# Performance work log

Hardware: AMD Instinct MI355X
Metric: run time of the kernel (lower is better)

Reference implementation:

```python
import jax, jax.numpy as jnp
import numpy as np

HIDDEN = 3072
N_HEADS = 16
Q_LORA = 1536
KV_LORA = 512
NOPE = 128
ROPE = 64
QK_HD = NOPE + ROPE  # 192
V_HD = 128
B, S = 2, 1024


def rms_norm(x, w, eps=1e-6):
    xf = x.astype(jnp.float32)
    var = jnp.mean(xf * xf, axis=-1, keepdims=True)
    return w * (xf * jax.lax.rsqrt(var + eps)).astype(x.dtype)


def apply_rope(x):
    # x: (b, s, h, d) with d even; interleaved pair rotation as in the source
    b, s, h, d = x.shape
    pos = jnp.arange(s, dtype=jnp.float32)
    inv_freq = 1.0 / (10000.0 ** (jnp.arange(0, d, 2, dtype=jnp.float32) / d))
    ang = pos[:, None] * inv_freq[None, :]          # (s, d/2)
    sin = jnp.sin(ang)[None, :, None, :]            # (1, s, 1, d/2)
    cos = jnp.cos(ang)[None, :, None, :]
    xr = x.reshape(b, s, h, d // 2, 2)
    x1, x2 = xr[..., 0], xr[..., 1]
    r1 = x1 * cos - x2 * sin
    r2 = x1 * sin + x2 * cos
    return jnp.stack([r1, r2], axis=-1).reshape(b, s, h, d)


def setup_inputs() -> dict:
    key = jax.random.key(0)
    ks = jax.random.split(key, 16)
    sc = 0.02
    inp = {
        "hidden_states": jax.random.normal(ks[0], (B, S, HIDDEN), jnp.float32),
        # causal additive mask (s, t): 0 on/below diagonal, -1e9 above
        "mask": jnp.where(jnp.tril(jnp.ones((S, S), bool)), 0.0, -1e9).astype(jnp.float32),
        "wq_a_w": jax.random.normal(ks[1], (Q_LORA, HIDDEN), jnp.float32) * sc,
        "wq_a_b": jnp.zeros((Q_LORA,), jnp.float32),
        "q_norm_w": jnp.ones((Q_LORA,), jnp.float32),
        "wq_b_w": jax.random.normal(ks[2], (HIDDEN, Q_LORA), jnp.float32) * sc,
        "wq_b_b": jnp.zeros((HIDDEN,), jnp.float32),
        "wkv_a_w": jax.random.normal(ks[3], (KV_LORA + ROPE, HIDDEN), jnp.float32) * sc,
        "wkv_a_b": jnp.zeros((KV_LORA + ROPE,), jnp.float32),
        "kv_norm_w": jnp.ones((KV_LORA,), jnp.float32),
        "wkv_b_w": jax.random.normal(ks[4], (N_HEADS * (NOPE + V_HD), KV_LORA), jnp.float32) * sc,
        "wkv_b_b": jnp.zeros((N_HEADS * (NOPE + V_HD),), jnp.float32),
        "wo_w": jax.random.normal(ks[5], (HIDDEN, N_HEADS * V_HD), jnp.float32) * sc,
        "wo_b": jnp.zeros((HIDDEN,), jnp.float32),
    }
    return inp


def reference(hidden_states, mask, wq_a_w, wq_a_b, q_norm_w, wq_b_w, wq_b_b,
              wkv_a_w, wkv_a_b, kv_norm_w, wkv_b_w, wkv_b_b, wo_w, wo_b):
    b, s, _ = hidden_states.shape
    scale = QK_HD ** (-0.5)

    # low-rank Q projection
    q_lat = hidden_states @ wq_a_w.T + wq_a_b                  # (b,s,q_lora)
    q = rms_norm(q_lat, q_norm_w) @ wq_b_w.T + wq_b_b          # (b,s,hidden)
    q = q.reshape(b, s, N_HEADS, QK_HD)
    q_nope, q_rope = q[..., :NOPE], q[..., NOPE:]
    q_rope = apply_rope(q_rope)
    q = jnp.concatenate([q_nope, q_rope], axis=-1)             # (b,s,h,192)

    # low-rank KV projection with decoupled rope key
    kv = hidden_states @ wkv_a_w.T + wkv_a_b                   # (b,s,kv_lora+rope)
    kv_lat, k_rope = kv[..., :KV_LORA], kv[..., KV_LORA:]
    k_rope = apply_rope(k_rope[:, :, None, :])                 # (b,s,1,64)
    kv = rms_norm(kv_lat, kv_norm_w) @ wkv_b_w.T + wkv_b_b
    kv = kv.reshape(b, s, N_HEADS, NOPE + V_HD)
    k_nope, v = kv[..., :NOPE], kv[..., NOPE:]
    k = jnp.concatenate([k_nope, jnp.broadcast_to(k_rope, (b, s, N_HEADS, ROPE))], axis=-1)

    # naive full attention, fp32 softmax (as in source)
    scores = jnp.einsum('bshd,bthd->bsht', q, k) * scale       # (b,s,h,t)
    scores = scores + mask[None, :, None, :]
    p = jax.nn.softmax(scores.astype(jnp.float32), axis=-1)
    out = jnp.einsum('bsht,bthd->bshd', p, v)                  # (b,s,h,v_hd)
    out = out.reshape(b, s, N_HEADS * V_HD)
    return out @ wo_w.T + wo_b
```

## Files before the change

kernel.cpp:

```cpp
#include <hip/hip_runtime.h>
#include <stdint.h>
#include <stddef.h>

#define NHEADS 16
#define QLORA  1536
#define KVLORA 512
#define QKH    192
#define VH     128
#define BB     2
#define SS     1024
#define MROWS  (BB*SS)
#define HID    3072

typedef __attribute__((ext_vector_type(4))) float fx4;
typedef __attribute__((ext_vector_type(4))) short sx4;
typedef __attribute__((ext_vector_type(8))) short sx8;

__device__ __forceinline__ short f2bf(float f) {
  uint32_t u = __builtin_bit_cast(uint32_t, f);
  u = (u + 0x7fffu + ((u >> 16) & 1u)) >> 16;
  return (short)u;
}
__device__ __forceinline__ float bf2f(short s) {
  uint32_t u = ((uint32_t)(uint16_t)s) << 16;
  return __builtin_bit_cast(float, u);
}
__device__ __forceinline__ void gl_lds16(const void* g, void* l) {
  __builtin_amdgcn_global_load_lds((const __attribute__((address_space(1))) void*)g,
                                   (__attribute__((address_space(3))) void*)l, 16, 0, 0);
}
__device__ __forceinline__ sx8 ldfrag(const short* p) {
  sx4 lo = *(const sx4*)p;
  sx4 hi = *(const sx4*)(p + 16);
  sx8 r;
  r[0]=lo[0]; r[1]=lo[1]; r[2]=lo[2]; r[3]=lo[3];
  r[4]=hi[0]; r[5]=hi[1]; r[6]=hi[2]; r[7]=hi[3];
  return r;
}
__device__ __forceinline__ sx8 ldfrag_swz(const short* lds, int row, int rowShorts,
                                          int baseChunk, int g) {
  const int r7 = row & 7;
  const int gh = g >> 1, lo4 = (g & 1) * 4;
  int ch0 = baseChunk + gh;
  int ch1 = baseChunk + 2 + gh;
  ch0 = (ch0 & ~7) | ((ch0 & 7) ^ r7);
  ch1 = (ch1 & ~7) | ((ch1 & 7) ^ r7);
  const short* base = lds + row * rowShorts;
  sx4 a = *(const sx4*)(base + ch0 * 8 + lo4);
  sx4 b = *(const sx4*)(base + ch1 * 8 + lo4);
  sx8 r;
  r[0]=a[0]; r[1]=a[1]; r[2]=a[2]; r[3]=a[3];
  r[4]=b[0]; r[5]=b[1]; r[6]=b[2]; r[7]=b[3];
  return r;
}
__device__ __forceinline__ sx8 ldfrag_swz32(const short* lds, int row, int g) {
  const int f = (row >> 1) & 3;
  const int c0 = (g >> 1) ^ f;
  const int c1 = (2 + (g >> 1)) ^ f;
  const int lo4 = (g & 1) * 4;
  const short* base = lds + row * 32;
  sx4 a = *(const sx4*)(base + c0 * 8 + lo4);
  sx4 b = *(const sx4*)(base + c1 * 8 + lo4);
  sx8 r;
  r[0]=a[0]; r[1]=a[1]; r[2]=a[2]; r[3]=a[3];
  r[4]=b[0]; r[5]=b[1]; r[6]=b[2]; r[7]=b[3];
  return r;
}

struct CvtSeg { const float* src; short* dst; int n4; };
__global__ void k_cvt6(CvtSeg s0, CvtSeg s1, CvtSeg s2, CvtSeg s3, CvtSeg s4, CvtSeg s5) {
  const CvtSeg segs[6] = {s0, s1, s2, s3, s4, s5};
  const int stride = gridDim.x * blockDim.x;
  const int t0 = blockIdx.x * blockDim.x + threadIdx.x;
#pragma unroll
  for (int s = 0; s < 6; ++s) {
    const float* src = segs[s].src;
    short* dst = segs[s].dst;
    const int n4 = segs[s].n4;
    for (int i = t0; i < n4; i += stride) {
      fx4 v = *(const fx4*)(src + (size_t)i * 4);
      sx4 o;
      o[0] = f2bf(v[0]); o[1] = f2bf(v[1]); o[2] = f2bf(v[2]); o[3] = f2bf(v[3]);
      *(sx4*)(dst + (size_t)i * 4) = o;
    }
  }
}

__global__ void k_rope_tab(float* __restrict__ tab) {
  int i = blockIdx.x * blockDim.x + threadIdx.x;
  if (i >= SS * 32) return;
  int pos = i >> 5, fi = i & 31;
  float inv = powf(10000.0f, -(float)fi / 32.0f);
  float ang = (float)pos * inv;
  tab[i * 2]     = cosf(ang);
  tab[i * 2 + 1] = sinf(ang);
}

struct GemmProb {
  const short* A; const short* Bt; const float* bias; void* C;
  int N; int K; int outbf16;
};

template <int MFR>
__global__ __launch_bounds__(256, 3)
void k_gemm2(GemmProb p0, GemmProb p1, int nblk0) {
  constexpr int TM = MFR * 32;
  constexpr int MT = 2048 / TM;
  int nwg = gridDim.x;
  int bid = (blockIdx.x % 8) * (nwg >> 3) + (blockIdx.x >> 3);
  const GemmProb p = (bid < nblk0) ? p0 : p1;
  int lb = (bid < nblk0) ? bid : bid - nblk0;
  const int m0 = (lb % MT) * TM;
  const int n0 = (lb / MT) * 128;

  __shared__ short As[2][TM * 32];
  __shared__ short Bs[2][128 * 32];
  const int tid  = threadIdx.x;
  const int lane = tid & 63;
  const int g    = lane >> 4;
  const int r16  = lane & 15;
  const int wave = tid >> 6;
  const int wm   = (wave >> 1) * (TM / 2);
  const int wn   = (wave & 1) * 64;
  const int N = p.N, K = p.K;

  fx4 acc[MFR][4] = {};

#define STAGE(bufi, kk)                                                        \
  do {                                                                         \
    _Pragma("unroll")                                                          \
    for (int i = 0; i < MFR / 2; ++i) {                                        \
      int cc = tid + 256 * i;                                                  \
      int row = cc >> 2;                                                       \
      int sc = ((cc & 3) ^ (row >> 1)) & 3;                                    \
      gl_lds16(p.A + (size_t)(m0 + row) * K + (kk) + sc * 8,                   \
               &As[bufi][cc * 8]);                                             \
    }                                                                          \
    _Pragma("unroll")                                                          \
    for (int i = 0; i < 2; ++i) {                                              \
      int cc = tid + 256 * i;                                                  \
      int row = cc >> 2;                                                       \
      int sc = ((cc & 3) ^ (row >> 1)) & 3;                                    \
      int bn = n0 + row; if (bn > N - 1) bn = N - 1;                           \
      gl_lds16(p.Bt + (size_t)bn * K + (kk) + sc * 8, &Bs[bufi][cc * 8]);      \
    }                                                                          \
  } while (0)

  const int nk = K >> 5;
  STAGE(0, 0);
  __syncthreads();

  int cur = 0;
  for (int t = 0; t < nk - 1; ++t) {
    STAGE(cur ^ 1, (t + 1) * 32);
    {
      sx8 af[MFR], bfv[4];
#pragma unroll
      for (int mi = 0; mi < MFR; ++mi)
        af[mi] = ldfrag_swz32(&As[cur][0], wm + mi * 16 + r16, g);
#pragma unroll
      for (int ni = 0; ni < 4; ++ni)
        bfv[ni] = ldfrag_swz32(&Bs[cur][0], wn + ni * 16 + r16, g);
#pragma unroll
      for (int mi = 0; mi < MFR; ++mi)
#pragma unroll
        for (int ni = 0; ni < 4; ++ni)
          acc[mi][ni] = __builtin_amdgcn_mfma_f32_16x16x32_bf16(af[mi], bfv[ni], acc[mi][ni], 0, 0, 0);
    }
    __syncthreads();
    cur ^= 1;
  }
  {
    sx8 af[MFR], bfv[4];
#pragma unroll
    for (int mi = 0; mi < MFR; ++mi)
      af[mi] = ldfrag_swz32(&As[cur][0], wm + mi * 16 + r16, g);
#pragma unroll
    for (int ni = 0; ni < 4; ++ni)
      bfv[ni] = ldfrag_swz32(&Bs[cur][0], wn + ni * 16 + r16, g);
#pragma unroll
    for (int mi = 0; mi < MFR; ++mi)
#pragma unroll
      for (int ni = 0; ni < 4; ++ni)
        acc[mi][ni] = __builtin_amdgcn_mfma_f32_16x16x32_bf16(af[mi], bfv[ni], acc[mi][ni], 0, 0, 0);
  }
#undef STAGE

  if (p.outbf16) {
#pragma unroll
    for (int mi = 0; mi < MFR; ++mi) {
      int mbase = m0 + wm + mi * 16 + 4 * g;
#pragma unroll
      for (int ni = 0; ni < 4; ++ni) {
        int ncol = n0 + wn + ni * 16 + r16;
        if (ncol < N) {
          float bv = p.bias[ncol];
#pragma unroll
          for (int r = 0; r < 4; ++r)
            ((short*)p.C)[(size_t)(mbase + r) * N + ncol] = f2bf(acc[mi][ni][r] + bv);
        }
      }
    }
  } else {
#pragma unroll
    for (int mi = 0; mi < MFR; ++mi) {
      int mbase = m0 + wm + mi * 16 + 4 * g;
#pragma unroll
      for (int ni = 0; ni < 4; ++ni) {
        int ncol = n0 + wn + ni * 16 + r16;
        if (ncol < N) {
          float bv = p.bias[ncol];
#pragma unroll
          for (int r = 0; r < 4; ++r)
            ((float*)p.C)[(size_t)(mbase + r) * N + ncol] = acc[mi][ni][r] + bv;
        }
      }
    }
  }
}

__global__ __launch_bounds__(256)
void k_prep(const short* __restrict__ qlat, const float* __restrict__ q_norm_w,
            short* __restrict__ qn,
            const short* __restrict__ kv, const float* __restrict__ kv_norm_w,
            short* __restrict__ kvn, short* __restrict__ kr,
            const float* __restrict__ tab) {
  const int row = blockIdx.x;
  const int t = threadIdx.x;
  const short* qr  = qlat + (size_t)row * QLORA;
  const short* kvr = kv + (size_t)row * 576;

  sx8 v;
  float s1 = 0.f, s2 = 0.f;
  if (t < 192) {
    v = *(const sx8*)(qr + t * 8);
#pragma unroll
    for (int j = 0; j < 8; ++j) { float f = bf2f(v[j]); s1 += f * f; }
  } else {
    v = *(const sx8*)(kvr + (t - 192) * 8);
#pragma unroll
    for (int j = 0; j < 8; ++j) { float f = bf2f(v[j]); s2 += f * f; }
  }
#pragma unroll
  for (int o = 32; o >= 1; o >>= 1) {
    s1 += __shfl_xor(s1, o, 64);
    s2 += __shfl_xor(s2, o, 64);
  }
  __shared__ float r1[4], r2[4];
  if ((t & 63) == 0) { r1[t >> 6] = s1; r2[t >> 6] = s2; }
  __syncthreads();
  float qss = r1[0] + r1[1] + r1[2] + r1[3];
  float kss = r2[0] + r2[1] + r2[2] + r2[3];
  float qrs = 1.0f / sqrtf(qss / (float)QLORA + 1e-6f);
  float krs = 1.0f / sqrtf(kss / (float)KVLORA + 1e-6f);

  if (t < 192) {
    sx8 o;
#pragma unroll
    for (int j = 0; j < 8; ++j) o[j] = f2bf(bf2f(v[j]) * qrs * q_norm_w[t * 8 + j]);
    *(sx8*)(qn + (size_t)row * QLORA + t * 8) = o;
  } else {
    int c = t - 192;
    sx8 o;
#pragma unroll
    for (int j = 0; j < 8; ++j) o[j] = f2bf(bf2f(v[j]) * krs * kv_norm_w[c * 8 + j]);
    *(sx8*)(kvn + (size_t)row * KVLORA + c * 8) = o;
  }
  if (t < 8) {
    sx8 x = *(const sx8*)(kvr + 512 + t * 8);
    int pos = row & (SS - 1);
    sx8 o;
#pragma unroll
    for (int k = 0; k < 4; ++k) {
      int i = t * 4 + k;
      float c = tab[(pos * 32 + i) * 2], s = tab[(pos * 32 + i) * 2 + 1];
      float x1 = bf2f(x[2 * k]), x2 = bf2f(x[2 * k + 1]);
      o[2 * k]     = f2bf(x1 * c - x2 * s);
      o[2 * k + 1] = f2bf(x1 * s + x2 * c);
    }
    *(sx8*)(kr + (size_t)row * 64 + t * 8) = o;
  }
}

__global__ __launch_bounds__(256)
void k_post(const short* __restrict__ kvb, short* __restrict__ vt,
            short* __restrict__ qb, const float* __restrict__ tab) {
  const int bid = blockIdx.x;
  const int tid = threadIdx.x;
  if (bid < 512) {
    const int bh = bid >> 4;
    const int t0 = (bid & 15) * 64;
    const int b = bh >> 4, h = bh & 15;
    __shared__ short sm[64 * 128];
#pragma unroll
    for (int i = 0; i < 4; ++i) {
      int c = tid + 256 * i;
      int tt = c >> 4, d0 = (c & 15) * 8;
      sx8 v = *(const sx8*)(kvb + ((size_t)(b * SS + t0 + tt)) * 4096 + h * 256 + 128 + d0);
      *(sx8*)(sm + tt * 128 + d0) = v;
    }
    __syncthreads();
#pragma unroll
    for (int i = 0; i < 4; ++i) {
      int c = tid + 256 * i;
      int d = c >> 3, tof = (c & 7) * 8;
      sx8 v;
#pragma unroll
      for (int j = 0; j < 8; ++j) v[j] = sm[(tof + j) * 128 + d];
      *(sx8*)(vt + ((size_t)bh * VH + d) * SS + t0 + tof) = v;
    }
  } else {
    int p = (bid - 512) * 256 + tid;
    int j = p & 7, h = (p >> 3) & 15, row = p >> 7;
    int pos = row & (SS - 1);
    size_t base = (((size_t)row * NHEADS + h) * QKH) + 128 + j * 8;
    sx8 x = *(const sx8*)(qb + base);
    sx8 o;
#pragma unroll
    for (int k = 0; k < 4; ++k) {
      int i = j * 4 + k;
      float c = tab[(pos * 32 + i) * 2], s = tab[(pos * 32 + i) * 2 + 1];
      float x1 = bf2f(x[2 * k]), x2 = bf2f(x[2 * k + 1]);
      o[2 * k]     = f2bf(x1 * c - x2 * s);
      o[2 * k + 1] = f2bf(x1 * s + x2 * c);
    }
    *(sx8*)(qb + base) = o;
  }
}

__global__ __launch_bounds__(256, 2)
void k_attn(const short* __restrict__ q, const short* __restrict__ kvb,
            const short* __restrict__ kr, const short* __restrict__ vt,
            short* __restrict__ ao) {
  const int bh = blockIdx.x;
  const int b = bh >> 4, h = bh & 15;
  const int qt0 = blockIdx.y * 64;
  const int tid = threadIdx.x;
  const int lane = tid & 63;
  const int wave = tid >> 6;
  const int g = lane >> 4, r16 = lane & 15;
  const int qg = qt0 + wave * 16 + r16;

  __shared__ short Ks[64 * QKH];
  __shared__ short Vs[VH * 64];

  sx8 qf[6];
  {
    const short* qr = q + (((size_t)(b * SS + qg)) * NHEADS + h) * QKH;
#pragma unroll
    for (int f = 0; f < 6; ++f) qf[f] = ldfrag(qr + f * 32 + 4 * g);
  }

  float mrun = -1e30f, lrun = 0.0f;
  fx4 oacc[8] = {};
  const float scale = 0.07216878364870323f;

  const int ntiles = qt0 / 64 + 1;
  for (int kt = 0; kt < ntiles; ++kt) {
    const int t0 = kt * 64;
#pragma unroll
    for (int i = 0; i < 6; ++i) {
      int cc = tid + 256 * i;
      int row = cc / 24, ch = cc % 24;
      int sc = (ch & 24) | ((ch & 7) ^ (row & 7));
      size_t grow = (size_t)(b * SS + t0 + row);
      const short* src = (sc < 16) ? kvb + grow * 4096 + h * 256 + sc * 8
                                   : kr + grow * 64 + (sc - 16) * 8;
      gl_lds16(src, &Ks[cc * 8]);
    }
#pragma unroll
    for (int i = 0; i < 4; ++i) {
      int cc = tid + 256 * i;
      int row = cc >> 3;
      int sc = (cc & 7) ^ (row & 7);
      gl_lds16(vt + ((size_t)bh * VH + row) * SS + t0 + sc * 8, &Vs[cc * 8]);
    }
    __syncthreads();

    const bool diag = (kt == ntiles - 1);
    float pv[16];
    float tmax = -1e30f;
#pragma unroll
    for (int th = 0; th < 4; ++th) {
      fx4 sacc = {};
#pragma unroll
      for (int f = 0; f < 6; ++f) {
        sx8 kf = ldfrag_swz(Ks, th * 16 + r16, QKH, f * 4, g);
        sacc = __builtin_amdgcn_mfma_f32_16x16x32_bf16(kf, qf[f], sacc, 0, 0, 0);
      }
#pragma unroll
      for (int r = 0; r < 4; ++r) {
        int t = t0 + th * 16 + 4 * g + r;
        float s = sacc[r] * scale;
        if (diag && t > qg) s = -1e30f;
        pv[th * 4 + r] = s;
        tmax = fmaxf(tmax, s);
      }
    }
    tmax = fmaxf(tmax, __shfl_xor(tmax, 16, 64));
    tmax = fmaxf(tmax, __shfl_xor(tmax, 32, 64));
    float mnew = fmaxf(mrun, tmax);
    float corr = __expf(mrun - mnew);
    float psum = 0.f;
#pragma unroll
    for (int j = 0; j < 16; ++j) { pv[j] = __expf(pv[j] - mnew); psum += pv[j]; }
    psum += __shfl_xor(psum, 16, 64);
    psum += __shfl_xor(psum, 32, 64);
    lrun = lrun * corr + psum;
    mrun = mnew;
#pragma unroll
    for (int f8 = 0; f8 < 8; ++f8) oacc[f8] *= corr;

    sx8 pf0, pf1;
#pragma unroll
    for (int j = 0; j < 8; ++j) { pf0[j] = f2bf(pv[j]); pf1[j] = f2bf(pv[8 + j]); }

#pragma unroll
    for (int f8 = 0; f8 < 8; ++f8) {
      sx8 v0 = ldfrag_swz(Vs, f8 * 16 + r16, 64, 0, g);
      sx8 v1 = ldfrag_swz(Vs, f8 * 16 + r16, 64, 4, g);
      oacc[f8] = __builtin_amdgcn_mfma_f32_16x16x32_bf16(v0, pf0, oacc[f8], 0, 0, 0);
      oacc[f8] = __builtin_amdgcn_mfma_f32_16x16x32_bf16(v1, pf1, oacc[f8], 0, 0, 0);
    }
    __syncthreads();
  }

  float inv = 1.0f / lrun;
#pragma unroll
  for (int f8 = 0; f8 < 8; ++f8)
#pragma unroll
    for (int r = 0; r < 4; ++r) {
      int d = f8 * 16 + 4 * g + r;
      ao[(((size_t)(b * SS + qg)) * NHEADS + h) * VH + d] = f2bf(oacc[f8][r] * inv);
    }
}

extern "C" void kernel_launch(void* const* d_in, const int* in_sizes, int n_in,
                              void* d_out, int out_size, void* d_ws, size_t ws_size,
                              hipStream_t stream) {
  const float* hs       = (const float*)d_in[0];
  const float* wq_a_w   = (const float*)d_in[2];
  const float* wq_a_b   = (const float*)d_in[3];
  const float* q_norm_w = (const float*)d_in[4];
  const float* wq_b_w   = (const float*)d_in[5];
  const float* wq_b_b   = (const float*)d_in[6];
  const float* wkv_a_w  = (const float*)d_in[7];
  const float* wkv_a_b  = (const float*)d_in[8];
  const float* kv_norm_w= (const float*)d_in[9];
  const float* wkv_b_w  = (const float*)d_in[10];
  const float* wkv_b_b  = (const float*)d_in[11];
  const float* wo_w     = (const float*)d_in[12];
  const float* wo_b     = (const float*)d_in[13];
  float* out = (float*)d_out;

  short* ws0 = (short*)d_ws;
  size_t off = 0;
  short* wqa_bf  = ws0 + off; off += (size_t)QLORA * HID;
  short* wqb_bf  = ws0 + off; off += (size_t)HID * QLORA;
  short* wkva_bf = ws0 + off; off += (size_t)576 * HID;
  short* wkvb_bf = ws0 + off; off += (size_t)4096 * KVLORA;
  short* wo_bf   = ws0 + off; off += (size_t)HID * 2048;
  short* h_bf    = ws0 + off; off += (size_t)MROWS * HID;
  short* qlat    = ws0 + off; off += (size_t)MROWS * QLORA;
  short* qn      = ws0 + off; off += (size_t)MROWS * QLORA;
  short* qb      = ws0 + off; off += (size_t)MROWS * HID;
  short* kv      = ws0 + off; off += (size_t)MROWS * 576;
  short* kr      = ws0 + off; off += (size_t)MROWS * 64;
  short* kvn     = ws0 + off; off += (size_t)MROWS * KVLORA;
  short* kvb     = ws0 + off; off += (size_t)MROWS * 4096;
  short* vtb     = ws0 + off; off += (size_t)BB * NHEADS * VH * SS;
  short* ao      = ws0 + off; off += (size_t)MROWS * 2048;
  float* tab     = (float*)(ws0 + off + (off & 1));

  {
    CvtSeg s0{wq_a_w,  wqa_bf,  (int)((size_t)QLORA * HID / 4)};
    CvtSeg s1{wq_b_w,  wqb_bf,  (int)((size_t)HID * QLORA / 4)};
    CvtSeg s2{wkv_a_w, wkva_bf, (int)((size_t)576 * HID / 4)};
    CvtSeg s3{wkv_b_w, wkvb_bf, (int)((size_t)4096 * KVLORA / 4)};
    CvtSeg s4{wo_w,    wo_bf,   (int)((size_t)HID * 2048 / 4)};
    CvtSeg s5{hs,      h_bf,    (int)((size_t)MROWS * HID / 4)};
    k_cvt6<<<2048, 256, 0, stream>>>(s0, s1, s2, s3, s4, s5);
  }
  k_rope_tab<<<(SS * 32 + 255) / 256, 256, 0, stream>>>(tab);

  {
    GemmProb pq{h_bf, wqa_bf,  wq_a_b,  qlat, QLORA, HID, 1};
    GemmProb pk{h_bf, wkva_bf, wkv_a_b, kv,   576,   HID, 1};
    int nb0 = 16 * (QLORA / 128);
    int nb1 = 16 * ((576 + 127) / 128);
    k_gemm2<4><<<nb0 + nb1, 256, 0, stream>>>(pq, pk, nb0);
  }

  k_prep<<<MROWS, 256, 0, stream>>>(qlat, q_norm_w, qn, kv, kv_norm_w, kvn, kr, tab);

  {
    GemmProb pq{qn,  wqb_bf,  wq_b_b,  qb,  HID,  QLORA,  1};
    GemmProb pk{kvn, wkvb_bf, wkv_b_b, kvb, 4096, KVLORA, 1};
    int nb0 = 16 * (HID / 128);
    int nb1 = 16 * (4096 / 128);
    k_gemm2<4><<<nb0 + nb1, 256, 0, stream>>>(pq, pk, nb0);
  }

  k_post<<<512 + 1024, 256, 0, stream>>>(kvb, vtb, qb, tab);

  k_attn<<<dim3(BB * NHEADS, SS / 64), 256, 0, stream>>>(qb, kvb, kr, vtb, ao);

  {
    GemmProb po{ao, wo_bf, wo_b, out, HID, 2048, 0};
    int nb0 = 32 * (HID / 128);
    k_gemm2<2><<<nb0, 256, 0, stream>>>(po, po, nb0);
  }
}
```

Measured before the change: 281.0 us.

## Add split-K to the first projection and output GEMMs with fused reduction

Adds a SPLITK template parameter to the GEMM kernel, which writes fp32 partial products into a workspace arena. The fused q_a/kv_a projection now splits K three ways, and the prep kernel sums the partials and adds the bias before the RMS norm and rope. The output projection moves from 64-row tiles to 128-row tiles with a 2-way split-K, and a new reduction kernel adds the partials plus the bias. The goal is more workgroups on the low-N, high-K GEMMs, at the cost of extra fp32 partial-sum traffic and one extra kernel launch.

```diff
diff --git a/kernel.cpp b/kernel.cpp
--- a/kernel.cpp
+++ b/kernel.cpp
@@ -98,11 +98,11 @@
 
 struct GemmProb {
   const short* A; const short* Bt; const float* bias; void* C;
-  int N; int K; int outbf16;
+  int N; int K;
 };
 
-template <int MFR>
-__global__ __launch_bounds__(256, 3)
+template <int MFR, int SPLITK>
+__global__ __launch_bounds__(256, 4)
 void k_gemm2(GemmProb p0, GemmProb p1, int nblk0) {
   constexpr int TM = MFR * 32;
   constexpr int MT = 2048 / TM;
@@ -110,8 +110,15 @@
   int bid = (blockIdx.x % 8) * (nwg >> 3) + (blockIdx.x >> 3);
   const GemmProb p = (bid < nblk0) ? p0 : p1;
   int lb = (bid < nblk0) ? bid : bid - nblk0;
-  const int m0 = (lb % MT) * TM;
-  const int n0 = (lb / MT) * 128;
+  const int N = p.N, K = p.K;
+  const int NT = (N + 127) >> 7;
+  const int tiles = MT * NT;
+  const int tile = lb % tiles;
+  const int pi = (SPLITK > 1) ? (lb / tiles) : 0;
+  const int m0 = (tile % MT) * TM;
+  const int n0 = (tile / MT) * 128;
+  const int Kc = K / SPLITK;
+  const int k0 = pi * Kc;
 
   __shared__ short As[2][TM * 32];
   __shared__ short Bs[2][128 * 32];
@@ -122,7 +129,6 @@
   const int wave = tid >> 6;
   const int wm   = (wave >> 1) * (TM / 2);
   const int wn   = (wave & 1) * 64;
-  const int N = p.N, K = p.K;
 
   fx4 acc[MFR][4] = {};
 
@@ -146,13 +152,13 @@
     }                                                                          \
   } while (0)
 
-  const int nk = K >> 5;
-  STAGE(0, 0);
+  const int nk = Kc >> 5;
+  STAGE(0, k0);
   __syncthreads();
 
   int cur = 0;
   for (int t = 0; t < nk - 1; ++t) {
-    STAGE(cur ^ 1, (t + 1) * 32);
+    STAGE(cur ^ 1, k0 + (t + 1) * 32);
     {
       sx8 af[MFR], bfv[4];
 #pragma unroll
@@ -186,7 +192,22 @@
   }
 #undef STAGE
 
-  if (p.outbf16) {
+  if (SPLITK > 1) {
+    float* Cp = (float*)p.C + (size_t)pi * 2048 * N;
+#pragma unroll
+    for (int mi = 0; mi < MFR; ++mi) {
+      int mbase = m0 + wm + mi * 16 + 4 * g;
+#pragma unroll
+      for (int ni = 0; ni < 4; ++ni) {
+        int ncol = n0 + wn + ni * 16 + r16;
+        if (ncol < N) {
+#pragma unroll
+          for (int r = 0; r < 4; ++r)
+            Cp[(size_t)(mbase + r) * N + ncol] = acc[mi][ni][r];
+        }
+      }
+    }
+  } else {
 #pragma unroll
     for (int mi = 0; mi < MFR; ++mi) {
       int mbase = m0 + wm + mi * 16 + 4 * g;
@@ -201,45 +222,47 @@
         }
       }
     }
-  } else {
-#pragma unroll
-    for (int mi = 0; mi < MFR; ++mi) {
-      int mbase = m0 + wm + mi * 16 + 4 * g;
-#pragma unroll
-      for (int ni = 0; ni < 4; ++ni) {
-        int ncol = n0 + wn + ni * 16 + r16;
-        if (ncol < N) {
-          float bv = p.bias[ncol];
-#pragma unroll
-          for (int r = 0; r < 4; ++r)
-            ((float*)p.C)[(size_t)(mbase + r) * N + ncol] = acc[mi][ni][r] + bv;
-        }
-      }
-    }
   }
 }
 
 __global__ __launch_bounds__(256)
-void k_prep(const short* __restrict__ qlat, const float* __restrict__ q_norm_w,
-            short* __restrict__ qn,
-            const short* __restrict__ kv, const float* __restrict__ kv_norm_w,
-            short* __restrict__ kvn, short* __restrict__ kr,
-            const float* __restrict__ tab) {
+void k_prep(const float* __restrict__ qp, const float* __restrict__ q_bias,
+            const float* __restrict__ q_norm_w, short* __restrict__ qn,
+            const float* __restrict__ kvp, const float* __restrict__ kv_bias,
+            const float* __restrict__ kv_norm_w, short* __restrict__ kvn,
+            short* __restrict__ kr, const float* __restrict__ tab) {
   const int row = blockIdx.x;
   const int t = threadIdx.x;
-  const short* qr  = qlat + (size_t)row * QLORA;
-  const short* kvr = kv + (size_t)row * 576;
-
-  sx8 v;
+  const size_t QS = (size_t)2048 * QLORA;
+  const size_t KS = (size_t)2048 * 576;
+
+  float x[8];
   float s1 = 0.f, s2 = 0.f;
   if (t < 192) {
-    v = *(const sx8*)(qr + t * 8);
-#pragma unroll
-    for (int j = 0; j < 8; ++j) { float f = bf2f(v[j]); s1 += f * f; }
+    const float* a = qp + (size_t)row * QLORA + t * 8;
+    fx4 u0 = *(const fx4*)(a),          u1 = *(const fx4*)(a + 4);
+    fx4 v0 = *(const fx4*)(a + QS),     v1 = *(const fx4*)(a + QS + 4);
+    fx4 w0 = *(const fx4*)(a + 2 * QS), w1 = *(const fx4*)(a + 2 * QS + 4);
+#pragma unroll
+    for (int j = 0; j < 4; ++j) {
+      x[j]     = u0[j] + v0[j] + w0[j] + q_bias[t * 8 + j];
+      x[4 + j] = u1[j] + v1[j] + w1[j] + q_bias[t * 8 + 4 + j];
+    }
+#pragma unroll
+    for (int j = 0; j < 8; ++j) s1 += x[j] * x[j];
   } else {
-    v = *(const sx8*)(kvr + (t - 192) * 8);
-#pragma unroll
-    for (int j = 0; j < 8; ++j) { float f = bf2f(v[j]); s2 += f * f; }
+    const int c = t - 192;
+    const float* a = kvp + (size_t)row * 576 + c * 8;
+    fx4 u0 = *(const fx4*)(a),          u1 = *(const fx4*)(a + 4);
+    fx4 v0 = *(const fx4*)(a + KS),     v1 = *(const fx4*)(a + KS + 4);
+    fx4 w0 = *(const fx4*)(a + 2 * KS), w1 = *(const fx4*)(a + 2 * KS + 4);
+#pragma unroll
+    for (int j = 0; j < 4; ++j) {
+      x[j]     = u0[j] + v0[j] + w0[j] + kv_bias[c * 8 + j];
+      x[4 + j] = u1[j] + v1[j] + w1[j] + kv_bias[c * 8 + 4 + j];
+    }
+#pragma unroll
+    for (int j = 0; j < 8; ++j) s2 += x[j] * x[j];
   }
 #pragma unroll
   for (int o = 32; o >= 1; o >>= 1) {
@@ -257,26 +280,34 @@
   if (t < 192) {
     sx8 o;
 #pragma unroll
-    for (int j = 0; j < 8; ++j) o[j] = f2bf(bf2f(v[j]) * qrs * q_norm_w[t * 8 + j]);
+    for (int j = 0; j < 8; ++j) o[j] = f2bf(x[j] * qrs * q_norm_w[t * 8 + j]);
     *(sx8*)(qn + (size_t)row * QLORA + t * 8) = o;
   } else {
     int c = t - 192;
     sx8 o;
 #pragma unroll
-    for (int j = 0; j < 8; ++j) o[j] = f2bf(bf2f(v[j]) * krs * kv_norm_w[c * 8 + j]);
+    for (int j = 0; j < 8; ++j) o[j] = f2bf(x[j] * krs * kv_norm_w[c * 8 + j]);
     *(sx8*)(kvn + (size_t)row * KVLORA + c * 8) = o;
   }
   if (t < 8) {
-    sx8 x = *(const sx8*)(kvr + 512 + t * 8);
+    const float* a = kvp + (size_t)row * 576 + 512 + t * 8;
+    fx4 u0 = *(const fx4*)(a),          u1 = *(const fx4*)(a + 4);
+    fx4 v0 = *(const fx4*)(a + KS),     v1 = *(const fx4*)(a + KS + 4);
+    fx4 w0 = *(const fx4*)(a + 2 * KS), w1 = *(const fx4*)(a + 2 * KS + 4);
+    float y[8];
+#pragma unroll
+    for (int j = 0; j < 4; ++j) {
+      y[j]     = u0[j] + v0[j] + w0[j] + kv_bias[512 + t * 8 + j];
+      y[4 + j] = u1[j] + v1[j] + w1[j] + kv_bias[512 + t * 8 + 4 + j];
+    }
     int pos = row & (SS - 1);
     sx8 o;
 #pragma unroll
     for (int k = 0; k < 4; ++k) {
       int i = t * 4 + k;
       float c = tab[(pos * 32 + i) * 2], s = tab[(pos * 32 + i) * 2 + 1];
-      float x1 = bf2f(x[2 * k]), x2 = bf2f(x[2 * k + 1]);
-      o[2 * k]     = f2bf(x1 * c - x2 * s);
-      o[2 * k + 1] = f2bf(x1 * s + x2 * c);
+      o[2 * k]     = f2bf(y[2 * k] * c - y[2 * k + 1] * s);
+      o[2 * k + 1] = f2bf(y[2 * k] * s + y[2 * k + 1] * c);
     }
     *(sx8*)(kr + (size_t)row * 64 + t * 8) = o;
   }
@@ -326,6 +357,19 @@
     }
     *(sx8*)(qb + base) = o;
   }
+}
+
+__global__ __launch_bounds__(256)
+void k_osum(const float* __restrict__ p, const float* __restrict__ bias,
+            float* __restrict__ out) {
+  const size_t OS = (size_t)2048 * HID;
+  int i = blockIdx.x * 256 + threadIdx.x;
+  fx4 a = *(const fx4*)(p + (size_t)i * 4);
+  fx4 b = *(const fx4*)(p + OS + (size_t)i * 4);
+  int col = (i * 4) % HID;
+  fx4 bv = *(const fx4*)(bias + col);
+  fx4 o = a + b + bv;
+  *(fx4*)(out + (size_t)i * 4) = o;
 }
 
 __global__ __launch_bounds__(256, 2)
@@ -461,16 +505,18 @@
   short* wkvb_bf = ws0 + off; off += (size_t)4096 * KVLORA;
   short* wo_bf   = ws0 + off; off += (size_t)HID * 2048;
   short* h_bf    = ws0 + off; off += (size_t)MROWS * HID;
-  short* qlat    = ws0 + off; off += (size_t)MROWS * QLORA;
   short* qn      = ws0 + off; off += (size_t)MROWS * QLORA;
+  short* kvn     = ws0 + off; off += (size_t)MROWS * KVLORA;
+  short* kr      = ws0 + off; off += (size_t)MROWS * 64;
   short* qb      = ws0 + off; off += (size_t)MROWS * HID;
-  short* kv      = ws0 + off; off += (size_t)MROWS * 576;
-  short* kr      = ws0 + off; off += (size_t)MROWS * 64;
-  short* kvn     = ws0 + off; off += (size_t)MROWS * KVLORA;
   short* kvb     = ws0 + off; off += (size_t)MROWS * 4096;
   short* vtb     = ws0 + off; off += (size_t)BB * NHEADS * VH * SS;
   short* ao      = ws0 + off; off += (size_t)MROWS * 2048;
   float* tab     = (float*)(ws0 + off + (off & 1));
+  float* arena   = tab + SS * 64;
+  float* qlatp   = arena;
+  float* kvp     = arena + (size_t)3 * 2048 * QLORA;
+  float* wop     = arena;
 
   {
     CvtSeg s0{wq_a_w,  wqa_bf,  (int)((size_t)QLORA * HID / 4)};
@@ -484,21 +530,22 @@
   k_rope_tab<<<(SS * 32 + 255) / 256, 256, 0, stream>>>(tab);
 
   {
-    GemmProb pq{h_bf, wqa_bf,  wq_a_b,  qlat, QLORA, HID, 1};
-    GemmProb pk{h_bf, wkva_bf, wkv_a_b, kv,   576,   HID, 1};
-    int nb0 = 16 * (QLORA / 128);
-    int nb1 = 16 * ((576 + 127) / 128);
-    k_gemm2<4><<<nb0 + nb1, 256, 0, stream>>>(pq, pk, nb0);
-  }
-
-  k_prep<<<MROWS, 256, 0, stream>>>(qlat, q_norm_w, qn, kv, kv_norm_w, kvn, kr, tab);
+    GemmProb pq{h_bf, wqa_bf,  nullptr, qlatp, QLORA, HID};
+    GemmProb pk{h_bf, wkva_bf, nullptr, kvp,   576,   HID};
+    int nb0 = 16 * (QLORA / 128) * 3;
+    int nb1 = 16 * ((576 + 127) / 128) * 3;
+    k_gemm2<4, 3><<<nb0 + nb1, 256, 0, stream>>>(pq, pk, nb0);
+  }
+
+  k_prep<<<MROWS, 256, 0, stream>>>(qlatp, wq_a_b, q_norm_w, qn,
+                                    kvp, wkv_a_b, kv_norm_w, kvn, kr, tab);
 
   {
-    GemmProb pq{qn,  wqb_bf,  wq_b_b,  qb,  HID,  QLORA,  1};
-    GemmProb pk{kvn, wkvb_bf, wkv_b_b, kvb, 4096, KVLORA, 1};
+    GemmProb pq{qn,  wqb_bf,  wq_b_b,  qb,  HID,  QLORA};
+    GemmProb pk{kvn, wkvb_bf, wkv_b_b, kvb, 4096, KVLORA};
     int nb0 = 16 * (HID / 128);
     int nb1 = 16 * (4096 / 128);
-    k_gemm2<4><<<nb0 + nb1, 256, 0, stream>>>(pq, pk, nb0);
+    k_gemm2<4, 1><<<nb0 + nb1, 256, 0, stream>>>(pq, pk, nb0);
   }
 
   k_post<<<512 + 1024, 256, 0, stream>>>(kvb, vtb, qb, tab);
@@ -506,8 +553,9 @@
   k_attn<<<dim3(BB * NHEADS, SS / 64), 256, 0, stream>>>(qb, kvb, kr, vtb, ao);
 
   {
-    GemmProb po{ao, wo_bf, wo_b, out, HID, 2048, 0};
-    int nb0 = 32 * (HID / 128);
-    k_gemm2<2><<<nb0, 256, 0, stream>>>(po, po, nb0);
-  }
-}
+    GemmProb po{ao, wo_bf, nullptr, wop, HID, 2048};
+    int nb = 16 * (HID / 128) * 2;
+    k_gemm2<4, 2><<<nb, 256, 0, stream>>>(po, po, nb);
+  }
+  k_osum<<<(MROWS * HID / 4) / 256, 256, 0, stream>>>(wop, wo_b, out);
+}
```

Result: faster. 253.1 us (-9.9%).
